# Kernel tuning notes

Measured on AMD Instinct MI355X. Metric: run time of the kernel, lower is better.

Reference implementation:

```python
import jax, jax.numpy as jnp
import numpy as np

IN, OUT, B = 8192, 8192, 256

def setup_inputs() -> dict:
    key = jax.random.key(0)
    k1, k2, k3, k4, k5 = jax.random.split(key, 5)
    x = jax.random.normal(k1, (B, IN), dtype=jnp.float32)
    low = jax.random.uniform(k2, (IN,), dtype=jnp.float32, minval=-1.0, maxval=0.0)
    high = low + jax.random.uniform(k3, (IN,), dtype=jnp.float32)  # guarantees low <= high
    W = jax.random.normal(k4, (OUT, IN), dtype=jnp.float32) * 0.02
    b = jax.random.normal(k5, (OUT,), dtype=jnp.float32) * 0.02
    return {"x": x, "low": low, "high": high, "W": W, "b": b}

def reference(x, low, high, W, b):
    # standard linear: x @ W.T + b
    y = jnp.einsum('bi,oi->bo', x, W) + b
    # interval bound propagation: swap bounds where weights are negative.
    # Equivalent to per-row masked matmul loop in the original:
    #   low_out[i]  = (W+[i] @ low) + (W-[i] @ high) + b[i]
    #   high_out[i] = (W+[i] @ high) + (W-[i] @ low) + b[i]
    W_pos = jnp.maximum(W, 0.0)
    W_neg = jnp.minimum(W, 0.0)
    low_out = W_pos @ low + W_neg @ high + b
    high_out = W_pos @ high + W_neg @ low + b
    return (y, low_out, high_out)
```

## Files before the change

kernel.cpp:

```cpp
#include <hip/hip_runtime.h>

#define M_TOTAL 256
#define N_TOTAL 8192
#define K_TOTAL 8192
#define TM 64
#define TN 64
#define BK 64
#define KITERS (K_TOTAL / BK)

typedef __attribute__((ext_vector_type(4))) float f32x4;
typedef __attribute__((ext_vector_type(8))) short s16x8;
typedef __attribute__((ext_vector_type(2))) int i32x2;

__device__ __forceinline__ int pk(float a, float b) {
    return (int)__builtin_amdgcn_perm(__float_as_uint(b), __float_as_uint(a), 0x07060302u);
}

__device__ __forceinline__ void barrier_lds() {
    asm volatile("s_waitcnt lgkmcnt(0)\n\ts_barrier" ::: "memory");
}

__global__ __launch_bounds__(256, 2)
void abstract_linear_kernel(const float* __restrict__ x,
                            const float* __restrict__ low,
                            const float* __restrict__ high,
                            const float* __restrict__ W,
                            const float* __restrict__ bias,
                            float* __restrict__ out) {
    __shared__ __align__(16) unsigned short As[2][TM * BK];
    __shared__ __align__(16) unsigned short Bs[2][TN * BK];

    const int t  = threadIdx.x;
    const int bx = blockIdx.x;
    const int n0 = (bx & 127) * TN;
    const int m_tile = bx >> 7;
    const int m0 = m_tile * TM;
    const bool do_bounds = (m_tile == 0);

    const int g  = t >> 4;
    const int sg = t & 15;

    const float* xg = x + (size_t)(m0 + g) * K_TOTAL + sg * 4;
    const float* wg = W + (size_t)(n0 + g) * K_TOTAL + sg * 4;
    const float* lg = low  + sg * 4;
    const float* hg = high + sg * 4;

    const int wave = t >> 6;
    const int lane = t & 63;
    const int wm  = wave >> 1;
    const int wn  = wave & 1;
    const int l15 = lane & 15;
    const int lq  = lane >> 4;

    f32x4 acc[2][2];
#pragma unroll
    for (int i = 0; i < 2; ++i)
#pragma unroll
        for (int j = 0; j < 2; ++j)
            acc[i][j] = (f32x4){0.f, 0.f, 0.f, 0.f};

    float P[4] = {0.f, 0.f, 0.f, 0.f};
    float R[4] = {0.f, 0.f, 0.f, 0.f};

    f32x4 a_reg[2][4], w_reg[2][4], lo_reg[2], hi_reg[2];

    auto issue = [&](int sl, int it) {
        const int kb = it * BK;
#pragma unroll
        for (int j = 0; j < 4; ++j)
            a_reg[sl][j] = *(const f32x4*)(xg + (size_t)j * 16 * K_TOTAL + kb);
#pragma unroll
        for (int j = 0; j < 4; ++j)
            w_reg[sl][j] = *(const f32x4*)(wg + (size_t)j * 16 * K_TOTAL + kb);
        if (do_bounds) {
            lo_reg[sl] = *(const f32x4*)(lg + kb);
            hi_reg[sl] = *(const f32x4*)(hg + kb);
        }
    };

    const int a_chunk = sg >> 1;
    const int a_half  = sg & 1;

    auto convert_write = [&](int sl, int buf) {
#pragma unroll
        for (int j = 0; j < 4; ++j) {
            f32x4 u = a_reg[sl][j];
            i32x2 d;
            d[0] = pk(u[0], u[1]);
            d[1] = pk(u[2], u[3]);
            int row = j * 16 + g;
            int pos = a_chunk ^ (row & 7);
            *(i32x2*)&As[buf][row * BK + pos * 8 + a_half * 4] = d;
        }
#pragma unroll
        for (int j = 0; j < 4; ++j) {
            f32x4 u = w_reg[sl][j];
            i32x2 d;
            d[0] = pk(u[0], u[1]);
            d[1] = pk(u[2], u[3]);
            int row = j * 16 + g;
            int pos = a_chunk ^ (row & 7);
            *(i32x2*)&Bs[buf][row * BK + pos * 8 + a_half * 4] = d;
        }
        if (do_bounds) {
            f32x4 l = lo_reg[sl], h = hi_reg[sl];
#pragma unroll
            for (int j = 0; j < 4; ++j) {
                f32x4 w = w_reg[sl][j];
#pragma unroll
                for (int e = 0; e < 4; ++e) {
                    float wv = w[e];
                    P[j] = fmaf(wv,        l[e] + h[e], P[j]);
                    R[j] = fmaf(fabsf(wv), h[e] - l[e], R[j]);
                }
            }
        }
    };

    auto mfma_tile = [&](int buf) {
#pragma unroll
        for (int s = 0; s < 2; ++s) {
            s16x8 af[2], bf[2];
#pragma unroll
            for (int mi = 0; mi < 2; ++mi) {
                int row = wm * 32 + mi * 16 + l15;
                int pos = (s * 4 + lq) ^ (row & 7);
                af[mi] = *(const s16x8*)&As[buf][row * BK + pos * 8];
            }
#pragma unroll
            for (int ni = 0; ni < 2; ++ni) {
                int row = wn * 32 + ni * 16 + l15;
                int pos = (s * 4 + lq) ^ (row & 7);
                bf[ni] = *(const s16x8*)&Bs[buf][row * BK + pos * 8];
            }
#pragma unroll
            for (int mi = 0; mi < 2; ++mi)
#pragma unroll
                for (int ni = 0; ni < 2; ++ni)
                    acc[mi][ni] = __builtin_amdgcn_mfma_f32_16x16x32_bf16(
                        af[mi], bf[ni], acc[mi][ni], 0, 0, 0);
        }
    };

    issue(0, 0);
    issue(1, 1);
    convert_write(0, 0);
    barrier_lds();

    for (int it = 0; it < KITERS - 2; it += 2) {
        issue(0, it + 2);
        mfma_tile(0);
        convert_write(1, 1);
        barrier_lds();

        issue(1, it + 3);
        mfma_tile(1);
        convert_write(0, 0);
        barrier_lds();
    }
    mfma_tile(0);
    convert_write(1, 1);
    barrier_lds();
    mfma_tile(1);

#pragma unroll
    for (int ni = 0; ni < 2; ++ni) {
        int go = n0 + wn * 32 + ni * 16 + l15;
        float bv = bias[go];
#pragma unroll
        for (int mi = 0; mi < 2; ++mi) {
            int gr = m0 + wm * 32 + mi * 16 + lq * 4;
#pragma unroll
            for (int r = 0; r < 4; ++r)
                out[(size_t)(gr + r) * N_TOTAL + go] = acc[mi][ni][r] + bv;
        }
    }

    if (do_bounds) {
#pragma unroll
        for (int j = 0; j < 4; ++j) {
            float p = P[j], r = R[j];
            p += __shfl_xor(p, 1);
            p += __shfl_xor(p, 2);
            p += __shfl_xor(p, 4);
            p += __shfl_xor(p, 8);
            r += __shfl_xor(r, 1);
            r += __shfl_xor(r, 2);
            r += __shfl_xor(r, 4);
            r += __shfl_xor(r, 8);
            if (sg == 0) {
                int o = n0 + j * 16 + g;
                float bv = bias[o];
                out[(size_t)M_TOTAL * N_TOTAL + o]           = 0.5f * (p - r) + bv;
                out[(size_t)M_TOTAL * N_TOTAL + N_TOTAL + o] = 0.5f * (p + r) + bv;
            }
        }
    }
}

extern "C" void kernel_launch(void* const* d_in, const int* in_sizes, int n_in,
                              void* d_out, int out_size, void* d_ws, size_t ws_size,
                              hipStream_t stream) {
    const float* x    = (const float*)d_in[0];
    const float* low  = (const float*)d_in[1];
    const float* high = (const float*)d_in[2];
    const float* W    = (const float*)d_in[3];
    const float* b    = (const float*)d_in[4];
    float* out = (float*)d_out;

    dim3 grid(4 * (N_TOTAL / TN));
    dim3 block(256);
    hipLaunchKernelGGL(abstract_linear_kernel, grid, block, 0, stream,
                       x, low, high, W, b, out);
}
```

Measured before the change: 440.8 us.

## Pre-pack x to bf16 fragments and stream W once per block with split-K

Adds a prep kernel that converts x to bf16 in an MFMA-fragment layout and precomputes low+high and high-low. The main kernel gives each block 32 output columns and all 256 rows. It loads W straight from global memory into registers as the MFMA B operand and splits K across 4 wave pairs, then reduces partial sums through LDS. This drops the LDS staging and barriers of the main loop and reads W only once, since the old grid re-read W for every M tile. In exchange there is an extra launch, a workspace round trip for x, only 256 blocks, and x fragments read from global/L2 on every K step.

```diff
diff --git a/kernel.cpp b/kernel.cpp
--- a/kernel.cpp
+++ b/kernel.cpp
@@ -3,198 +3,157 @@
 #define M_TOTAL 256
 #define N_TOTAL 8192
 #define K_TOTAL 8192
-#define TM 64
-#define TN 64
-#define BK 64
-#define KITERS (K_TOTAL / BK)
 
 typedef __attribute__((ext_vector_type(4))) float f32x4;
 typedef __attribute__((ext_vector_type(8))) short s16x8;
-typedef __attribute__((ext_vector_type(2))) int i32x2;
+typedef __attribute__((ext_vector_type(4))) int   i32x4;
+typedef unsigned short ushort_t;
 
 __device__ __forceinline__ int pk(float a, float b) {
     return (int)__builtin_amdgcn_perm(__float_as_uint(b), __float_as_uint(a), 0x07060302u);
 }
 
-__device__ __forceinline__ void barrier_lds() {
-    asm volatile("s_waitcnt lgkmcnt(0)\n\ts_barrier" ::: "memory");
+__global__ __launch_bounds__(256)
+void prep_kernel(const float* __restrict__ x,
+                 const float* __restrict__ low,
+                 const float* __restrict__ high,
+                 ushort_t* __restrict__ xpre,
+                 float* __restrict__ lh,
+                 float* __restrict__ hl) {
+    const int bx = blockIdx.x, t = threadIdx.x;
+    if (bx < 1024) {
+        const int id  = bx * 256 + t;
+        const int kt  = id >> 11;
+        const int c   = (id >> 8) & 7;
+        const int row = id & 255;
+        const float* src = x + (size_t)row * K_TOTAL + kt * 64 + c * 8;
+        f32x4 s0 = *(const f32x4*)(src);
+        f32x4 s1 = *(const f32x4*)(src + 4);
+        i32x4 bi;
+        bi[0] = pk(s0[0], s0[1]); bi[1] = pk(s0[2], s0[3]);
+        bi[2] = pk(s1[0], s1[1]); bi[3] = pk(s1[2], s1[3]);
+        *(i32x4*)(xpre + (size_t)id * 8) = bi;
+    } else {
+        const int i = (bx - 1024) * 256 + t;
+        float lo = low[i], hi = high[i];
+        lh[i] = lo + hi;
+        hl[i] = hi - lo;
+    }
 }
 
-__global__ __launch_bounds__(256, 2)
-void abstract_linear_kernel(const float* __restrict__ x,
-                            const float* __restrict__ low,
-                            const float* __restrict__ high,
+__global__ __launch_bounds__(512)
+void abstract_linear_kernel(const ushort_t* __restrict__ xpre,
                             const float* __restrict__ W,
+                            const float* __restrict__ lh,
+                            const float* __restrict__ hl,
                             const float* __restrict__ bias,
                             float* __restrict__ out) {
-    __shared__ __align__(16) unsigned short As[2][TM * BK];
-    __shared__ __align__(16) unsigned short Bs[2][TN * BK];
+    __shared__ float ybuf[M_TOTAL * 32];
+    __shared__ float pbuf[4 * 32];
+    __shared__ float rbuf[4 * 32];
 
-    const int t  = threadIdx.x;
-    const int bx = blockIdx.x;
-    const int n0 = (bx & 127) * TN;
-    const int m_tile = bx >> 7;
-    const int m0 = m_tile * TM;
-    const bool do_bounds = (m_tile == 0);
+    const int t    = threadIdx.x;
+    const int w    = t >> 6;
+    const int nw   = w & 1;
+    const int kh   = w >> 1;
+    const int lane = t & 63;
+    const int l15  = lane & 15;
+    const int lq   = lane >> 4;
+    const int n0   = blockIdx.x * 32;
+    const int nl   = nw * 16 + l15;
 
-    const int g  = t >> 4;
-    const int sg = t & 15;
+    f32x4 acc[16];
+#pragma unroll
+    for (int i = 0; i < 16; ++i) acc[i] = (f32x4){0.f, 0.f, 0.f, 0.f};
 
-    const float* xg = x + (size_t)(m0 + g) * K_TOTAL + sg * 4;
-    const float* wg = W + (size_t)(n0 + g) * K_TOTAL + sg * 4;
-    const float* lg = low  + sg * 4;
-    const float* hg = high + sg * 4;
+    float P = 0.f, R = 0.f;
 
-    const int wave = t >> 6;
-    const int lane = t & 63;
-    const int wm  = wave >> 1;
-    const int wn  = wave & 1;
-    const int l15 = lane & 15;
-    const int lq  = lane >> 4;
+    const float*    wp  = W  + (size_t)(n0 + nl) * K_TOTAL + kh * 2048 + lq * 8;
+    const float*    lhp = lh + kh * 2048 + lq * 8;
+    const float*    hlp = hl + kh * 2048 + lq * 8;
+    const ushort_t* ap  = xpre + (size_t)kh * 64 * 8192 + lq * 2048 + l15 * 8;
 
-    f32x4 acc[2][2];
+    f32x4 wA[2], wB[2], lA[2], lB[2], hA[2], hB[2];
+
+    auto ldW = [&](int sl, int st) {
+        wA[sl] = *(const f32x4*)(wp  + st * 32);
+        wB[sl] = *(const f32x4*)(wp  + st * 32 + 4);
+        lA[sl] = *(const f32x4*)(lhp + st * 32);
+        lB[sl] = *(const f32x4*)(lhp + st * 32 + 4);
+        hA[sl] = *(const f32x4*)(hlp + st * 32);
+        hB[sl] = *(const f32x4*)(hlp + st * 32 + 4);
+    };
+
+    auto compute = [&](int sl, int st) {
+        f32x4 w0 = wA[sl], w1 = wB[sl];
+        i32x4 bi;
+        bi[0] = pk(w0[0], w0[1]); bi[1] = pk(w0[2], w0[3]);
+        bi[2] = pk(w1[0], w1[1]); bi[3] = pk(w1[2], w1[3]);
+        s16x8 bf = *(s16x8*)&bi;
+        f32x4 l0 = lA[sl], l1 = lB[sl], h0 = hA[sl], h1 = hB[sl];
 #pragma unroll
-    for (int i = 0; i < 2; ++i)
+        for (int e = 0; e < 4; ++e) {
+            P = fmaf(w0[e], l0[e], P);
+            P = fmaf(w1[e], l1[e], P);
+            R = fmaf(fabsf(w0[e]), h0[e], R);
+            R = fmaf(fabsf(w1[e]), h1[e], R);
+        }
+        const ushort_t* a_st = ap + (size_t)st * 8192;
 #pragma unroll
-        for (int j = 0; j < 2; ++j)
-            acc[i][j] = (f32x4){0.f, 0.f, 0.f, 0.f};
-
-    float P[4] = {0.f, 0.f, 0.f, 0.f};
-    float R[4] = {0.f, 0.f, 0.f, 0.f};
-
-    f32x4 a_reg[2][4], w_reg[2][4], lo_reg[2], hi_reg[2];
-
-    auto issue = [&](int sl, int it) {
-        const int kb = it * BK;
+        for (int half = 0; half < 2; ++half) {
+            s16x8 af[8];
 #pragma unroll
-        for (int j = 0; j < 4; ++j)
-            a_reg[sl][j] = *(const f32x4*)(xg + (size_t)j * 16 * K_TOTAL + kb);
+            for (int mi = 0; mi < 8; ++mi)
+                af[mi] = *(const s16x8*)(a_st + (half * 8 + mi) * 128);
 #pragma unroll
-        for (int j = 0; j < 4; ++j)
-            w_reg[sl][j] = *(const f32x4*)(wg + (size_t)j * 16 * K_TOTAL + kb);
-        if (do_bounds) {
-            lo_reg[sl] = *(const f32x4*)(lg + kb);
-            hi_reg[sl] = *(const f32x4*)(hg + kb);
+            for (int mi = 0; mi < 8; ++mi)
+                acc[half * 8 + mi] = __builtin_amdgcn_mfma_f32_16x16x32_bf16(
+                    af[mi], bf, acc[half * 8 + mi], 0, 0, 0);
         }
     };
 
-    const int a_chunk = sg >> 1;
-    const int a_half  = sg & 1;
+    ldW(0, 0);
+    for (int st = 0; st < 64; st += 2) {
+        ldW(1, st + 1);
+        compute(0, st);
+        if (st < 62) ldW(0, st + 2);
+        compute(1, st + 1);
+    }
 
-    auto convert_write = [&](int sl, int buf) {
+    P += __shfl_xor(P, 16); P += __shfl_xor(P, 32);
+    R += __shfl_xor(R, 16); R += __shfl_xor(R, 32);
+    if (lane < 16) {
+        pbuf[kh * 32 + nl] = P;
+        rbuf[kh * 32 + nl] = R;
+    }
+
+    const float bv = bias[n0 + nl];
+
+    for (int rr = 0; rr < 4; ++rr) {
+        __syncthreads();
+        if (kh == rr) {
 #pragma unroll
-        for (int j = 0; j < 4; ++j) {
-            f32x4 u = a_reg[sl][j];
-            i32x2 d;
-            d[0] = pk(u[0], u[1]);
-            d[1] = pk(u[2], u[3]);
-            int row = j * 16 + g;
-            int pos = a_chunk ^ (row & 7);
-            *(i32x2*)&As[buf][row * BK + pos * 8 + a_half * 4] = d;
-        }
-#pragma unroll
-        for (int j = 0; j < 4; ++j) {
-            f32x4 u = w_reg[sl][j];
-            i32x2 d;
-            d[0] = pk(u[0], u[1]);
-            d[1] = pk(u[2], u[3]);
-            int row = j * 16 + g;
-            int pos = a_chunk ^ (row & 7);
-            *(i32x2*)&Bs[buf][row * BK + pos * 8 + a_half * 4] = d;
-        }
-        if (do_bounds) {
-            f32x4 l = lo_reg[sl], h = hi_reg[sl];
-#pragma unroll
-            for (int j = 0; j < 4; ++j) {
-                f32x4 w = w_reg[sl][j];
+            for (int mi = 0; mi < 16; ++mi) {
 #pragma unroll
                 for (int e = 0; e < 4; ++e) {
-                    float wv = w[e];
-                    P[j] = fmaf(wv,        l[e] + h[e], P[j]);
-                    R[j] = fmaf(fabsf(wv), h[e] - l[e], R[j]);
+                    int m = mi * 16 + lq * 4 + e;
+                    int idx = m * 32 + nl;
+                    float v = acc[mi][e];
+                    if (rr > 0) v += ybuf[idx];
+                    if (rr < 3) ybuf[idx] = v;
+                    else out[(size_t)m * N_TOTAL + n0 + nl] = v + bv;
                 }
             }
         }
-    };
+    }
+    __syncthreads();
 
-    auto mfma_tile = [&](int buf) {
-#pragma unroll
-        for (int s = 0; s < 2; ++s) {
-            s16x8 af[2], bf[2];
-#pragma unroll
-            for (int mi = 0; mi < 2; ++mi) {
-                int row = wm * 32 + mi * 16 + l15;
-                int pos = (s * 4 + lq) ^ (row & 7);
-                af[mi] = *(const s16x8*)&As[buf][row * BK + pos * 8];
-            }
-#pragma unroll
-            for (int ni = 0; ni < 2; ++ni) {
-                int row = wn * 32 + ni * 16 + l15;
-                int pos = (s * 4 + lq) ^ (row & 7);
-                bf[ni] = *(const s16x8*)&Bs[buf][row * BK + pos * 8];
-            }
-#pragma unroll
-            for (int mi = 0; mi < 2; ++mi)
-#pragma unroll
-                for (int ni = 0; ni < 2; ++ni)
-                    acc[mi][ni] = __builtin_amdgcn_mfma_f32_16x16x32_bf16(
-                        af[mi], bf[ni], acc[mi][ni], 0, 0, 0);
-        }
-    };
-
-    issue(0, 0);
-    issue(1, 1);
-    convert_write(0, 0);
-    barrier_lds();
-
-    for (int it = 0; it < KITERS - 2; it += 2) {
-        issue(0, it + 2);
-        mfma_tile(0);
-        convert_write(1, 1);
-        barrier_lds();
-
-        issue(1, it + 3);
-        mfma_tile(1);
-        convert_write(0, 0);
-        barrier_lds();
-    }
-    mfma_tile(0);
-    convert_write(1, 1);
-    barrier_lds();
-    mfma_tile(1);
-
-#pragma unroll
-    for (int ni = 0; ni < 2; ++ni) {
-        int go = n0 + wn * 32 + ni * 16 + l15;
-        float bv = bias[go];
-#pragma unroll
-        for (int mi = 0; mi < 2; ++mi) {
-            int gr = m0 + wm * 32 + mi * 16 + lq * 4;
-#pragma unroll
-            for (int r = 0; r < 4; ++r)
-                out[(size_t)(gr + r) * N_TOTAL + go] = acc[mi][ni][r] + bv;
-        }
-    }
-
-    if (do_bounds) {
-#pragma unroll
-        for (int j = 0; j < 4; ++j) {
-            float p = P[j], r = R[j];
-            p += __shfl_xor(p, 1);
-            p += __shfl_xor(p, 2);
-            p += __shfl_xor(p, 4);
-            p += __shfl_xor(p, 8);
-            r += __shfl_xor(r, 1);
-            r += __shfl_xor(r, 2);
-            r += __shfl_xor(r, 4);
-            r += __shfl_xor(r, 8);
-            if (sg == 0) {
-                int o = n0 + j * 16 + g;
-                float bv = bias[o];
-                out[(size_t)M_TOTAL * N_TOTAL + o]           = 0.5f * (p - r) + bv;
-                out[(size_t)M_TOTAL * N_TOTAL + N_TOTAL + o] = 0.5f * (p + r) + bv;
-            }
-        }
+    if (w == 0 && lane < 32) {
+        float Ps = pbuf[lane] + pbuf[32 + lane] + pbuf[64 + lane] + pbuf[96 + lane];
+        float Rs = rbuf[lane] + rbuf[32 + lane] + rbuf[64 + lane] + rbuf[96 + lane];
+        float bb = bias[n0 + lane];
+        out[(size_t)M_TOTAL * N_TOTAL + n0 + lane]           = 0.5f * (Ps - Rs) + bb;
+        out[(size_t)M_TOTAL * N_TOTAL + N_TOTAL + n0 + lane] = 0.5f * (Ps + Rs) + bb;
     }
 }
 
@@ -208,8 +167,12 @@
     const float* b    = (const float*)d_in[4];
     float* out = (float*)d_out;
 
-    dim3 grid(4 * (N_TOTAL / TN));
-    dim3 block(256);
-    hipLaunchKernelGGL(abstract_linear_kernel, grid, block, 0, stream,
-                       x, low, high, W, b, out);
+    ushort_t* xpre = (ushort_t*)d_ws;
+    float* lh = (float*)((char*)d_ws + (size_t)M_TOTAL * K_TOTAL * 2);
+    float* hl = lh + K_TOTAL;
+
+    hipLaunchKernelGGL(prep_kernel, dim3(1056), dim3(256), 0, stream,
+                       x, low, high, xpre, lh, hl);
+    hipLaunchKernelGGL(abstract_linear_kernel, dim3(N_TOTAL / 32), dim3(512), 0, stream,
+                       xpre, W, lh, hl, b, out);
 }
```

After: 484.1 us. 1.1x slower.
